# Performance work log

Measured on AMD Instinct MI355X. Metric: run time of the kernel, lower is better.

## Reference

```python
import jax, jax.numpy as jnp
import numpy as np

B, S, F, DK = 8, 2048, 1024, 128

def setup_inputs() -> dict:
    key = jax.random.key(0)
    ks = jax.random.split(key, 6)
    scale = 0.02
    return {
        "q": jax.random.normal(ks[0], (B, S, F), dtype=jnp.float32),
        "k": jax.random.normal(ks[1], (B, S, F), dtype=jnp.float32),
        "v": jax.random.normal(ks[2], (B, S, F), dtype=jnp.float32),
        "w_q": jax.random.normal(ks[3], (F, DK), dtype=jnp.float32) * scale,
        "w_k": jax.random.normal(ks[4], (F, DK), dtype=jnp.float32) * scale,
        "w_v": jax.random.normal(ks[5], (F, DK), dtype=jnp.float32) * scale,
    }

def reference(q, k, v, w_q, w_k, w_v):
    d_k = w_q.shape[-1]
    # bias-free linear projections: [B,S,F] @ [F,DK] -> [B,S,DK]
    qp = jnp.einsum("bsf,fd->bsd", q, w_q)
    kp = jnp.einsum("bsf,fd->bsd", k, w_k)
    vp = jnp.einsum("bsf,fd->bsd", v, w_v)
    # scaled dot-product scores: [B,S,S]
    scores = jnp.einsum("bqd,bkd->bqk", qp, kp) * (1.0 / jnp.sqrt(jnp.float32(d_k)))
    attn = jax.nn.softmax(scores, axis=-1)
    out = jnp.einsum("bqk,bkd->bqd", attn, vp)
    return out
```

## Files before the change

kernel.cpp:

```cpp
#include <hip/hip_runtime.h>
#include <hip/hip_bf16.h>

#define B_ 8
#define S_ 2048
#define F_ 1024
#define DK_ 128
#define M_ (B_*S_)

typedef unsigned short u16;
typedef short short8 __attribute__((ext_vector_type(8)));
typedef float f32x4 __attribute__((ext_vector_type(4)));
typedef float f32x16 __attribute__((ext_vector_type(16)));

__device__ __forceinline__ u16 f2bf(float f) {
    unsigned int u = __float_as_uint(f);
    u += 0x7FFFu + ((u >> 16) & 1u);
    return (u16)(u >> 16);
}
__device__ __forceinline__ unsigned int pack2(float a, float b) {
    return (unsigned int)f2bf(a) | ((unsigned int)f2bf(b) << 16);
}
__device__ __forceinline__ float fexp2(float x) {
#if __has_builtin(__builtin_amdgcn_exp2f)
    return __builtin_amdgcn_exp2f(x);
#else
    return exp2f(x);
#endif
}
__device__ __forceinline__ unsigned int cvt_pk_bf16(float lo, float hi) {
    unsigned int r;
    asm volatile("v_cvt_pk_bf16_f32 %0, %1, %2" : "=v"(r) : "v"(lo), "v"(hi));
    return r;
}
__device__ __forceinline__ void pl32_swap(unsigned int& a, unsigned int& b) {
    asm volatile("v_permlane32_swap_b32 %0, %1" : "+v"(a), "+v"(b));
}

__global__ __launch_bounds__(256) void prep_wt(const float* __restrict__ wq,
                                               const float* __restrict__ wk,
                                               const float* __restrict__ wv,
                                               u16* __restrict__ WT) {
    int id = blockIdx.x * 256 + threadIdx.x;
    if (id >= 3 * DK_ * F_) return;
    int m   = id / (DK_ * F_);
    int rem = id - m * (DK_ * F_);
    int c   = rem / F_;
    int k   = rem - c * F_;
    const float* w = (m == 0) ? wq : (m == 1) ? wk : wv;
    float v = w[k * DK_ + c];
    if (m == 0) v *= 0.12751741951f;
    WT[id] = f2bf(v);
}

__global__ __launch_bounds__(256, 3) void proj(const float* __restrict__ xq,
                                               const float* __restrict__ xk,
                                               const float* __restrict__ xv,
                                               const u16* __restrict__ WT,
                                               u16* __restrict__ qp,
                                               u16* __restrict__ kp,
                                               u16* __restrict__ vpT) {
    const int mode = blockIdx.y;
    const float* X = (mode == 0) ? xq : (mode == 1) ? xk : xv;
    const u16*   W = WT + mode * (DK_ * F_);

    __shared__ u16 a_lds[64][40];
    __shared__ u16 w_lds[128][40];

    const int t    = threadIdx.x;
    const int lane = t & 63;
    const int wv_  = t >> 6;
    const int l15  = lane & 15, l4 = lane >> 4;
    const int row0 = blockIdx.x * 64;

    f32x4 acc[8];
#pragma unroll
    for (int j = 0; j < 8; ++j) acc[j] = f32x4{0.f, 0.f, 0.f, 0.f};

    for (int k0 = 0; k0 < F_; k0 += 32) {
        {
            int r = t >> 2, kk = (t & 3) * 8;
            const float4* src = (const float4*)(X + (size_t)(row0 + r) * F_ + k0 + kk);
            float4 f0 = src[0], f1 = src[1];
            int4 o0;
            o0.x = pack2(f0.x, f0.y); o0.y = pack2(f0.z, f0.w);
            o0.z = pack2(f1.x, f1.y); o0.w = pack2(f1.z, f1.w);
            *(int4*)&a_lds[r][kk] = o0;
        }
        {
            int c = t >> 1, kk = (t & 1) * 16;
            const int4* src = (const int4*)(W + (size_t)c * F_ + k0 + kk);
            *(int4*)&w_lds[c][kk]     = src[0];
            *(int4*)&w_lds[c][kk + 8] = src[1];
        }
        __syncthreads();

        short8 af = *(const short8*)&a_lds[wv_ * 16 + l15][l4 * 8];
        short8 bf[8];
#pragma unroll
        for (int ct = 0; ct < 8; ++ct)
            bf[ct] = *(const short8*)&w_lds[ct * 16 + l15][l4 * 8];

        if (mode < 2) {
#pragma unroll
            for (int ct = 0; ct < 8; ++ct)
                acc[ct] = __builtin_amdgcn_mfma_f32_16x16x32_bf16(af, bf[ct], acc[ct], 0, 0, 0);
        } else {
#pragma unroll
            for (int ct = 0; ct < 8; ++ct)
                acc[ct] = __builtin_amdgcn_mfma_f32_16x16x32_bf16(bf[ct], af, acc[ct], 0, 0, 0);
        }
        __syncthreads();
    }

    if (mode < 2) {
        u16* OUT = (mode == 0) ? qp : kp;
#pragma unroll
        for (int ct = 0; ct < 8; ++ct)
#pragma unroll
            for (int r = 0; r < 4; ++r) {
                int row = row0 + wv_ * 16 + l4 * 4 + r;
                int col = ct * 16 + l15;
                OUT[(size_t)row * DK_ + col] = f2bf(acc[ct][r]);
            }
    } else {
#pragma unroll
        for (int ct = 0; ct < 8; ++ct)
#pragma unroll
            for (int r = 0; r < 4; ++r) {
                int n = ct * 16 + l4 * 4 + r;
                int m = row0 + wv_ * 16 + l15;
                vpT[(size_t)n * M_ + m] = f2bf(acc[ct][r]);
            }
    }
}

union attn_lds_t {
    struct {
        __align__(16) unsigned char kbuf[2][16384];
        __align__(16) unsigned char vbuf[2][16384];
    } s;
    struct { float ob[32][132]; } e;
};

__global__ __launch_bounds__(256, 2) void attn(const u16* __restrict__ qp,
                                               const u16* __restrict__ kp,
                                               const u16* __restrict__ vpT,
                                               float* __restrict__ out) {
    __shared__ attn_lds_t u;
    __shared__ float m_lds[2][32], l_lds[2][2][32], gm_lds[32], gl_lds[32];

    const int t      = threadIdx.x;
    const int lane   = t & 63;
    const int wv_    = t >> 6;
    const int kv_sub = wv_ & 1;
    const int d_half = wv_ >> 1;
    const int r31    = lane & 31;
    const int hi     = lane >> 5;

    const int b  = blockIdx.x & 7;
    const int qi = blockIdx.x >> 3;
    const int qrow0 = b * S_ + qi * 32;
    const int kvb0  = b * S_;

    short8 qf[8];
#pragma unroll
    for (int c = 0; c < 8; ++c)
        qf[c] = *(const short8*)(qp + (size_t)(qrow0 + r31) * DK_ + c * 16 + hi * 8);

    f32x16 o4[2];
#pragma unroll
    for (int ct = 0; ct < 2; ++ct)
#pragma unroll
        for (int i = 0; i < 16; ++i) o4[ct][i] = 0.f;
    float mrun = -1.0e30f, lrun = 0.f;

    int4 gk[4], gv[4];
    int kr[4], kc[4], vr[4], vc[4];
#pragma unroll
    for (int j = 0; j < 4; ++j) {
        int f = t + 256 * j;
        kr[j] = f >> 4; kc[j] = f & 15;
        vr[j] = f >> 3; vc[j] = f & 7;
    }

#define LOADT(kvb)                                                                \
    {                                                                             \
        _Pragma("unroll")                                                         \
        for (int j = 0; j < 4; ++j) {                                             \
            gk[j] = *(const int4*)(kp + (size_t)((kvb) + kr[j]) * DK_ + kc[j] * 8);\
            gv[j] = *(const int4*)(vpT + (size_t)vr[j] * M_ + (kvb) + vc[j] * 8); \
        }                                                                         \
    }
#define WRITET(nb)                                                                \
    {                                                                             \
        _Pragma("unroll")                                                         \
        for (int j = 0; j < 4; ++j) {                                             \
            *(int4*)(u.s.kbuf[nb] + kr[j] * 256 + ((kc[j] ^ (kr[j] & 15)) << 4)) = gk[j]; \
            *(int4*)(u.s.vbuf[nb] + vr[j] * 128 + ((vc[j] ^ (vr[j] & 7)) << 4)) = gv[j];  \
        }                                                                         \
    }

    LOADT(kvb0);
    WRITET(0);
    int cur = 0;

    for (int kt = 0; kt < 32; ++kt) {
        __syncthreads();

        if (kt < 31) LOADT(kvb0 + (kt + 1) * 64);

        const unsigned char* kb = u.s.kbuf[cur];
        const unsigned char* vb = u.s.vbuf[cur];

        const int krow  = kv_sub * 32 + r31;
        const int kbase = krow * 256;
        const int ksw   = krow & 15;
        short8 kf[8];
#pragma unroll
        for (int c = 0; c < 8; ++c)
            kf[c] = *(const short8*)(kb + kbase + (((c * 2 + hi) ^ ksw) << 4));

        f32x16 sa, sb;
#pragma unroll
        for (int i = 0; i < 16; ++i) { sa[i] = 0.f; sb[i] = 0.f; }
#pragma unroll
        for (int c = 0; c < 4; ++c) {
            sa = __builtin_amdgcn_mfma_f32_32x32x16_bf16(kf[c],     qf[c],     sa, 0, 0, 0);
            sb = __builtin_amdgcn_mfma_f32_32x32x16_bf16(kf[c + 4], qf[c + 4], sb, 0, 0, 0);
        }
        f32x16 st;
#pragma unroll
        for (int i = 0; i < 16; ++i) st[i] = sa[i] + sb[i];

        float tm = st[0];
#pragma unroll
        for (int i = 1; i < 16; ++i) tm = fmaxf(tm, st[i]);
        if (__any(tm > mrun + 8.0f)) {
            tm = fmaxf(tm, __shfl_xor(tm, 32, 64));
            float mn = fmaxf(mrun, tm);
            float fs = fexp2(mrun - mn);
            mrun = mn;
            lrun *= fs;
#pragma unroll
            for (int ct = 0; ct < 2; ++ct)
#pragma unroll
                for (int i = 0; i < 16; ++i) o4[ct][i] *= fs;
        }
        float s0 = 0.f, s1 = 0.f;
#pragma unroll
        for (int i = 0; i < 16; i += 2) {
            st[i]     = fexp2(st[i] - mrun);
            st[i + 1] = fexp2(st[i + 1] - mrun);
            s0 += st[i]; s1 += st[i + 1];
        }
        lrun += s0 + s1;

        short8 bp[2];
#pragma unroll
        for (int ch = 0; ch < 2; ++ch) {
            unsigned int A1 = cvt_pk_bf16(st[ch * 8 + 0], st[ch * 8 + 1]);
            unsigned int A2 = cvt_pk_bf16(st[ch * 8 + 2], st[ch * 8 + 3]);
            unsigned int A3 = cvt_pk_bf16(st[ch * 8 + 4], st[ch * 8 + 5]);
            unsigned int A4 = cvt_pk_bf16(st[ch * 8 + 6], st[ch * 8 + 7]);
            pl32_swap(A1, A3);
            pl32_swap(A2, A4);
            int4 w;
            w.x = (int)A1; w.y = (int)A2; w.z = (int)A3; w.w = (int)A4;
            bp[ch] = *(short8*)&w;
        }

        if (kt < 31) WRITET(cur ^ 1);

#pragma unroll
        for (int ct = 0; ct < 2; ++ct) {
            const int vrow  = d_half * 64 + ct * 32 + r31;
            const int vbase = vrow * 128;
            const int vsw   = vrow & 7;
#pragma unroll
            for (int ch = 0; ch < 2; ++ch) {
                short8 vf = *(const short8*)(vb + vbase
                                             + (((kv_sub * 4 + ch * 2 + hi) ^ vsw) << 4));
                o4[ct] = __builtin_amdgcn_mfma_f32_32x32x16_bf16(vf, bp[ch], o4[ct], 0, 0, 0);
            }
        }

        cur ^= 1;
    }
#undef LOADT
#undef WRITET

    __syncthreads();
    if (d_half == 0) {
        l_lds[kv_sub][hi][r31] = lrun;
        if (lane < 32) m_lds[kv_sub][r31] = mrun;
    }
    __syncthreads();
    if (t < 32) {
        float m0 = m_lds[0][t], m1 = m_lds[1][t];
        float gm = fmaxf(m0, m1);
        float gl = (l_lds[0][0][t] + l_lds[0][1][t]) * fexp2(m0 - gm)
                 + (l_lds[1][0][t] + l_lds[1][1][t]) * fexp2(m1 - gm);
        gm_lds[t] = gm;
        gl_lds[t] = gl;
    }
    __syncthreads();

    const float sc = fexp2(mrun - gm_lds[r31]);
    if (kv_sub == 0) {
#pragma unroll
        for (int ct = 0; ct < 2; ++ct)
#pragma unroll
            for (int i = 0; i < 16; ++i) {
                int d = d_half * 64 + ct * 32 + (i & 3) + 8 * (i >> 2) + 4 * hi;
                u.e.ob[r31][d] = o4[ct][i] * sc;
            }
    }
    __syncthreads();
    if (kv_sub == 1) {
#pragma unroll
        for (int ct = 0; ct < 2; ++ct)
#pragma unroll
            for (int i = 0; i < 16; ++i) {
                int d = d_half * 64 + ct * 32 + (i & 3) + 8 * (i >> 2) + 4 * hi;
                u.e.ob[r31][d] += o4[ct][i] * sc;
            }
    }
    __syncthreads();

    {
        int row = t >> 3, d0 = (t & 7) * 16;
        float inv = 1.0f / gl_lds[row];
        float* dst = out + (size_t)(qrow0 + row) * DK_ + d0;
#pragma unroll
        for (int j = 0; j < 16; j += 4) {
            float4 v;
            v.x = u.e.ob[row][d0 + j]     * inv;
            v.y = u.e.ob[row][d0 + j + 1] * inv;
            v.z = u.e.ob[row][d0 + j + 2] * inv;
            v.w = u.e.ob[row][d0 + j + 3] * inv;
            *(float4*)(dst + j) = v;
        }
    }
}

extern "C" void kernel_launch(void* const* d_in, const int* in_sizes, int n_in,
                              void* d_out, int out_size, void* d_ws, size_t ws_size,
                              hipStream_t stream) {
    const float* q  = (const float*)d_in[0];
    const float* k  = (const float*)d_in[1];
    const float* v  = (const float*)d_in[2];
    const float* wq = (const float*)d_in[3];
    const float* wk = (const float*)d_in[4];
    const float* wv = (const float*)d_in[5];
    float* out = (float*)d_out;

    char* ws = (char*)d_ws;
    u16* WT  = (u16*)ws;
    u16* qp  = (u16*)(ws + 786432);
    u16* kp  = (u16*)(ws + 786432 + 4194304);
    u16* vpT = (u16*)(ws + 786432 + 2 * 4194304);

    prep_wt<<<dim3(1536), dim3(256), 0, stream>>>(wq, wk, wv, WT);
    proj<<<dim3(256, 3), dim3(256), 0, stream>>>(q, k, v, WT, qp, kp, vpT);
    attn<<<dim3(512), dim3(256), 0, stream>>>(qp, kp, vpT, out);
}
```

Before: 85.88 us.

## Enlarge attention tile to 64 queries and 128-key stages with 8 waves

The attention kernel now uses 512-thread blocks covering 64 query rows, with each wave computing all 128 output columns for its 32 queries over one of four 32-key sub-slices of a 128-key stage. Each staged K/V tile is therefore reused by twice as many queries, which halves global K/V traffic, and there are half as many loop iterations and barriers. The load and LDS write are fused into a single STAGE step issued before compute, and the inline asm loses its volatile qualifier so the compiler can schedule it. The costs are 128KB of LDS and 4 output accumulators per wave (more register pressure), only 256 blocks, one block per CU, and a serialized four-way reduction at the end.

After: 76.41 us. 1.12x faster.

```diff
diff --git a/kernel.cpp b/kernel.cpp
--- a/kernel.cpp
+++ b/kernel.cpp
@@ -29,11 +29,11 @@
 }
 __device__ __forceinline__ unsigned int cvt_pk_bf16(float lo, float hi) {
     unsigned int r;
-    asm volatile("v_cvt_pk_bf16_f32 %0, %1, %2" : "=v"(r) : "v"(lo), "v"(hi));
+    asm("v_cvt_pk_bf16_f32 %0, %1, %2" : "=v"(r) : "v"(lo), "v"(hi));
     return r;
 }
 __device__ __forceinline__ void pl32_swap(unsigned int& a, unsigned int& b) {
-    asm volatile("v_permlane32_swap_b32 %0, %1" : "+v"(a), "+v"(b));
+    asm("v_permlane32_swap_b32 %0, %1" : "+v"(a), "+v"(b));
 }
 
 __global__ __launch_bounds__(256) void prep_wt(const float* __restrict__ wq,
@@ -136,89 +136,84 @@
 
 union attn_lds_t {
     struct {
-        __align__(16) unsigned char kbuf[2][16384];
-        __align__(16) unsigned char vbuf[2][16384];
+        __align__(16) unsigned char kbuf[2][32768];
+        __align__(16) unsigned char vbuf[2][32768];
     } s;
-    struct { float ob[32][132]; } e;
+    struct { float ob[64][132]; } e;
 };
 
-__global__ __launch_bounds__(256, 2) void attn(const u16* __restrict__ qp,
+__global__ __launch_bounds__(512, 1) void attn(const u16* __restrict__ qp,
                                                const u16* __restrict__ kp,
                                                const u16* __restrict__ vpT,
                                                float* __restrict__ out) {
     __shared__ attn_lds_t u;
-    __shared__ float m_lds[2][32], l_lds[2][2][32], gm_lds[32], gl_lds[32];
+    __shared__ float m_l[2][4][32], l_l[2][4][2][32], gm_l[2][32], gl_l[2][32];
 
     const int t      = threadIdx.x;
     const int lane   = t & 63;
     const int wv_    = t >> 6;
-    const int kv_sub = wv_ & 1;
-    const int d_half = wv_ >> 1;
+    const int q_sub  = wv_ & 1;
+    const int kv_sub = wv_ >> 1;
     const int r31    = lane & 31;
     const int hi     = lane >> 5;
 
     const int b  = blockIdx.x & 7;
     const int qi = blockIdx.x >> 3;
-    const int qrow0 = b * S_ + qi * 32;
+    const int qrow0 = b * S_ + qi * 64;
     const int kvb0  = b * S_;
 
     short8 qf[8];
 #pragma unroll
     for (int c = 0; c < 8; ++c)
-        qf[c] = *(const short8*)(qp + (size_t)(qrow0 + r31) * DK_ + c * 16 + hi * 8);
-
-    f32x16 o4[2];
-#pragma unroll
-    for (int ct = 0; ct < 2; ++ct)
+        qf[c] = *(const short8*)(qp + (size_t)(qrow0 + q_sub * 32 + r31) * DK_
+                                    + c * 16 + hi * 8);
+
+    f32x16 o4[4];
+#pragma unroll
+    for (int ct = 0; ct < 4; ++ct)
 #pragma unroll
         for (int i = 0; i < 16; ++i) o4[ct][i] = 0.f;
     float mrun = -1.0e30f, lrun = 0.f;
 
-    int4 gk[4], gv[4];
-    int kr[4], kc[4], vr[4], vc[4];
+    int kr[4], kc[4];
 #pragma unroll
     for (int j = 0; j < 4; ++j) {
-        int f = t + 256 * j;
+        int f = t + 512 * j;
         kr[j] = f >> 4; kc[j] = f & 15;
-        vr[j] = f >> 3; vc[j] = f & 7;
-    }
-
-#define LOADT(kvb)                                                                \
+    }
+
+#define STAGE(kvb, nb)                                                            \
     {                                                                             \
+        int4 gk[4], gv[4];                                                        \
         _Pragma("unroll")                                                         \
         for (int j = 0; j < 4; ++j) {                                             \
             gk[j] = *(const int4*)(kp + (size_t)((kvb) + kr[j]) * DK_ + kc[j] * 8);\
-            gv[j] = *(const int4*)(vpT + (size_t)vr[j] * M_ + (kvb) + vc[j] * 8); \
+            gv[j] = *(const int4*)(vpT + (size_t)kr[j] * M_ + (kvb) + kc[j] * 8); \
         }                                                                         \
-    }
-#define WRITET(nb)                                                                \
-    {                                                                             \
         _Pragma("unroll")                                                         \
         for (int j = 0; j < 4; ++j) {                                             \
             *(int4*)(u.s.kbuf[nb] + kr[j] * 256 + ((kc[j] ^ (kr[j] & 15)) << 4)) = gk[j]; \
-            *(int4*)(u.s.vbuf[nb] + vr[j] * 128 + ((vc[j] ^ (vr[j] & 7)) << 4)) = gv[j];  \
+            *(int4*)(u.s.vbuf[nb] + kr[j] * 256 + ((kc[j] ^ (kr[j] & 15)) << 4)) = gv[j]; \
         }                                                                         \
     }
 
-    LOADT(kvb0);
-    WRITET(0);
+    STAGE(kvb0, 0);
     int cur = 0;
 
-    for (int kt = 0; kt < 32; ++kt) {
+    for (int kt = 0; kt < 16; ++kt) {
         __syncthreads();
 
-        if (kt < 31) LOADT(kvb0 + (kt + 1) * 64);
+        if (kt < 15) STAGE(kvb0 + (kt + 1) * 128, cur ^ 1);
 
         const unsigned char* kb = u.s.kbuf[cur];
         const unsigned char* vb = u.s.vbuf[cur];
 
-        const int krow  = kv_sub * 32 + r31;
-        const int kbase = krow * 256;
-        const int ksw   = krow & 15;
+        const int krow = kv_sub * 32 + r31;
+        const int ksw  = krow & 15;
         short8 kf[8];
 #pragma unroll
         for (int c = 0; c < 8; ++c)
-            kf[c] = *(const short8*)(kb + kbase + (((c * 2 + hi) ^ ksw) << 4));
+            kf[c] = *(const short8*)(kb + krow * 256 + (((c * 2 + hi) ^ ksw) << 4));
 
         f32x16 sa, sb;
 #pragma unroll
@@ -242,7 +237,7 @@
             mrun = mn;
             lrun *= fs;
 #pragma unroll
-            for (int ct = 0; ct < 2; ++ct)
+            for (int ct = 0; ct < 4; ++ct)
 #pragma unroll
                 for (int i = 0; i < 16; ++i) o4[ct][i] *= fs;
         }
@@ -269,16 +264,13 @@
             bp[ch] = *(short8*)&w;
         }
 
-        if (kt < 31) WRITET(cur ^ 1);
-
-#pragma unroll
-        for (int ct = 0; ct < 2; ++ct) {
-            const int vrow  = d_half * 64 + ct * 32 + r31;
-            const int vbase = vrow * 128;
-            const int vsw   = vrow & 7;
+#pragma unroll
+        for (int ct = 0; ct < 4; ++ct) {
+            const int vrow = ct * 32 + r31;
+            const int vsw  = vrow & 15;
 #pragma unroll
             for (int ch = 0; ch < 2; ++ch) {
-                short8 vf = *(const short8*)(vb + vbase
+                short8 vf = *(const short8*)(vb + vrow * 256
                                              + (((kv_sub * 4 + ch * 2 + hi) ^ vsw) << 4));
                 o4[ct] = __builtin_amdgcn_mfma_f32_32x32x16_bf16(vf, bp[ch], o4[ct], 0, 0, 0);
             }
@@ -286,50 +278,54 @@
 
         cur ^= 1;
     }
-#undef LOADT
-#undef WRITET
+#undef STAGE
 
     __syncthreads();
-    if (d_half == 0) {
-        l_lds[kv_sub][hi][r31] = lrun;
-        if (lane < 32) m_lds[kv_sub][r31] = mrun;
-    }
+    l_l[q_sub][kv_sub][hi][r31] = lrun;
+    if (lane < 32) m_l[q_sub][kv_sub][r31] = mrun;
     __syncthreads();
-    if (t < 32) {
-        float m0 = m_lds[0][t], m1 = m_lds[1][t];
-        float gm = fmaxf(m0, m1);
-        float gl = (l_lds[0][0][t] + l_lds[0][1][t]) * fexp2(m0 - gm)
-                 + (l_lds[1][0][t] + l_lds[1][1][t]) * fexp2(m1 - gm);
-        gm_lds[t] = gm;
-        gl_lds[t] = gl;
+    if (t < 64) {
+        int qs = t >> 5, qq = t & 31;
+        float gm = -1.0e30f;
+#pragma unroll
+        for (int ks = 0; ks < 4; ++ks) gm = fmaxf(gm, m_l[qs][ks][qq]);
+        float gl = 0.f;
+#pragma unroll
+        for (int ks = 0; ks < 4; ++ks)
+            gl += (l_l[qs][ks][0][qq] + l_l[qs][ks][1][qq]) * fexp2(m_l[qs][ks][qq] - gm);
+        gm_l[qs][qq] = gm;
+        gl_l[qs][qq] = gl;
     }
     __syncthreads();
 
-    const float sc = fexp2(mrun - gm_lds[r31]);
-    if (kv_sub == 0) {
-#pragma unroll
-        for (int ct = 0; ct < 2; ++ct)
-#pragma unroll
-            for (int i = 0; i < 16; ++i) {
-                int d = d_half * 64 + ct * 32 + (i & 3) + 8 * (i >> 2) + 4 * hi;
-                u.e.ob[r31][d] = o4[ct][i] * sc;
+    const float sc = fexp2(mrun - gm_l[q_sub][r31]);
+    const int qrow = q_sub * 32 + r31;
+    for (int rr = 0; rr < 4; ++rr) {
+        if (kv_sub == rr) {
+            if (rr == 0) {
+#pragma unroll
+                for (int ct = 0; ct < 4; ++ct)
+#pragma unroll
+                    for (int i = 0; i < 16; ++i) {
+                        int d = ct * 32 + (i & 3) + 8 * (i >> 2) + 4 * hi;
+                        u.e.ob[qrow][d] = o4[ct][i] * sc;
+                    }
+            } else {
+#pragma unroll
+                for (int ct = 0; ct < 4; ++ct)
+#pragma unroll
+                    for (int i = 0; i < 16; ++i) {
+                        int d = ct * 32 + (i & 3) + 8 * (i >> 2) + 4 * hi;
+                        u.e.ob[qrow][d] += o4[ct][i] * sc;
+                    }
             }
-    }
-    __syncthreads();
-    if (kv_sub == 1) {
-#pragma unroll
-        for (int ct = 0; ct < 2; ++ct)
-#pragma unroll
-            for (int i = 0; i < 16; ++i) {
-                int d = d_half * 64 + ct * 32 + (i & 3) + 8 * (i >> 2) + 4 * hi;
-                u.e.ob[r31][d] += o4[ct][i] * sc;
-            }
-    }
-    __syncthreads();
+        }
+        __syncthreads();
+    }
 
     {
         int row = t >> 3, d0 = (t & 7) * 16;
-        float inv = 1.0f / gl_lds[row];
+        float inv = 1.0f / gl_l[row >> 5][row & 31];
         float* dst = out + (size_t)(qrow0 + row) * DK_ + d0;
 #pragma unroll
         for (int j = 0; j < 16; j += 4) {
@@ -362,5 +358,5 @@
 
     prep_wt<<<dim3(1536), dim3(256), 0, stream>>>(wq, wk, wv, WT);
     proj<<<dim3(256, 3), dim3(256), 0, stream>>>(q, k, v, WT, qp, kp, vpT);
-    attn<<<dim3(512), dim3(256), 0, stream>>>(qp, kp, vpT, out);
-}
+    attn<<<dim3(256), dim3(512), 0, stream>>>(qp, kp, vpT, out);
+}
```
